# Kernel optimization log

Hardware: AMD Instinct MI355X
Metric: run time of the kernel (lower is better)

## Reference

```python
import jax, jax.numpy as jnp
import numpy as np

N, E, F_IN, H, G, C = 50000, 600000, 128, 128, 500, 10


def _lin(k, fi, fo):
    # Glorot-ish scaled init for a [fi, fo] weight
    return (jax.random.normal(k, (fi, fo), jnp.float32) / np.float32(np.sqrt(fi)))


def setup_inputs() -> dict:
    key = jax.random.key(0)
    ks = jax.random.split(key, 16)
    x = jax.random.normal(ks[0], (N, F_IN), jnp.float32)
    edge_index = jax.random.randint(ks[1], (2, E), 0, N, dtype=jnp.int32)
    batch = jnp.sort(jax.random.randint(ks[2], (N,), 0, G, dtype=jnp.int32))
    return {
        "x": x, "edge_index": edge_index, "batch": batch,
        # SAGEConv i: out = mean_aggr @ Wl + bl + x @ Wr  (PyG default: mean aggr, root weight, bias on lin_l)
        "Wl1": _lin(ks[3], F_IN, H), "bl1": jnp.zeros((H,), jnp.float32), "Wr1": _lin(ks[4], F_IN, H),
        "Wl2": _lin(ks[5], H, H),    "bl2": jnp.zeros((H,), jnp.float32), "Wr2": _lin(ks[6], H, H),
        "Wl3": _lin(ks[7], H, H),    "bl3": jnp.zeros((H,), jnp.float32), "Wr3": _lin(ks[8], H, H),
        "W4": _lin(ks[9], H, 64), "b4": jnp.zeros((64,), jnp.float32),
        "W5": _lin(ks[10], 64, C), "b5": jnp.zeros((C,), jnp.float32),
    }


def _segment_mean(vals, ids, num_segments):
    s = jax.ops.segment_sum(vals, ids, num_segments=num_segments)
    cnt = jax.ops.segment_sum(jnp.ones((vals.shape[0], 1), vals.dtype), ids, num_segments=num_segments)
    return s / jnp.maximum(cnt, 1.0)


def _sage_conv(x, src, dst, Wl, bl, Wr):
    # gather source features along edges, mean-aggregate at destinations
    aggr = _segment_mean(x[src], dst, N)  # [N, F]
    return aggr @ Wl + bl + x @ Wr


def reference(x, edge_index, batch, Wl1, bl1, Wr1, Wl2, bl2, Wr2, Wl3, bl3, Wr3, W4, b4, W5, b5):
    src, dst = edge_index[0], edge_index[1]
    h = jax.nn.relu(_sage_conv(x, src, dst, Wl1, bl1, Wr1))
    h = jax.nn.relu(_sage_conv(h, src, dst, Wl2, bl2, Wr2))
    h = jax.nn.relu(_sage_conv(h, src, dst, Wl3, bl3, Wr3))
    g = _segment_mean(h, batch, G)          # global mean pool -> [G, H]
    g = jax.nn.relu(g @ W4 + b4)
    return jax.nn.log_softmax(g @ W5 + b5, axis=-1)
```

## Files before the change

kernel.cpp:

```cpp
#include <hip/hip_runtime.h>
#include <hip/hip_bf16.h>
#include <math.h>

#define FH 128

typedef __attribute__((ext_vector_type(8))) short short8v;
typedef __attribute__((ext_vector_type(4))) float float4v;
typedef unsigned short ushort_t;
typedef unsigned int   uint32;

__device__ __forceinline__ ushort_t f2bf(float f) {
    uint32 u = __builtin_bit_cast(uint32, f);
    u += 0x7fffu + ((u >> 16) & 1u);
    return (ushort_t)(u >> 16);
}
__device__ __forceinline__ float bf_lo(uint32 w) { return __builtin_bit_cast(float, w << 16); }
__device__ __forceinline__ float bf_hi(uint32 w) { return __builtin_bit_cast(float, w & 0xffff0000u); }
__device__ __forceinline__ uint32 pack2(float lo, float hi) {
    return (uint32)f2bf(lo) | ((uint32)f2bf(hi) << 16);
}

__global__ __launch_bounds__(256) void zero_kernel(int* __restrict__ p, int n) {
    int i = (blockIdx.x * 256 + threadIdx.x) * 4;
    if (i + 3 < n) {
        *(int4*)(p + i) = make_int4(0, 0, 0, 0);
    } else {
        for (int j = i; j < n; ++j) p[j] = 0;
    }
}

__device__ __forceinline__ void pack_one(const float* __restrict__ Wl,
                                         const float* __restrict__ Wr,
                                         ushort_t* __restrict__ Bp, int t) {
    int k = t >> 7, n = t & 127;
    float v = (k < FH) ? Wl[k * FH + n] : Wr[(k - FH) * FH + n];
    int nt = n >> 4, kt = k >> 5;
    int lane = (n & 15) + (((k >> 3) & 3) << 4);
    int j = k & 7;
    Bp[(((nt * 8 + kt) * 64) + lane) * 8 + j] = f2bf(v);
}

__global__ __launch_bounds__(256) void fused_prep_kernel(
        const float* __restrict__ x, ushort_t* __restrict__ xb, size_t n, int cvtBlocks,
        const float* __restrict__ Wl1, const float* __restrict__ Wr1, ushort_t* __restrict__ Bp1,
        const float* __restrict__ Wl2, const float* __restrict__ Wr2, ushort_t* __restrict__ Bp2,
        const float* __restrict__ Wl3, const float* __restrict__ Wr3, ushort_t* __restrict__ Bp3,
        const int* __restrict__ dst, int* __restrict__ deg, int E, int degBlocks,
        const int* __restrict__ batch, int* __restrict__ gstart, int N, int G) {
    int b = blockIdx.x;
    if (b < cvtBlocks) {
        size_t base = ((size_t)b * 256 + threadIdx.x) * 8;
        if (base >= n) return;
        const float4 a = *(const float4*)(x + base);
        const float4 c = *(const float4*)(x + base + 4);
        ushort_t o[8] = {f2bf(a.x), f2bf(a.y), f2bf(a.z), f2bf(a.w),
                         f2bf(c.x), f2bf(c.y), f2bf(c.z), f2bf(c.w)};
        *(uint4*)(xb + base) = *(const uint4*)o;
        return;
    }
    b -= cvtBlocks;
    if (b < 384) {
        int which = b >> 7;
        int t = (b & 127) * 256 + threadIdx.x;
        if (which == 0)      pack_one(Wl1, Wr1, Bp1, t);
        else if (which == 1) pack_one(Wl2, Wr2, Bp2, t);
        else                 pack_one(Wl3, Wr3, Bp3, t);
        return;
    }
    b -= 384;
    if (b < degBlocks) {
        int e = b * 256 + threadIdx.x;
        if (e < E) atomicAdd(&deg[dst[e]], 1);
        return;
    }
    b -= degBlocks;
    {
        int g = b * 256 + threadIdx.x;
        if (g > G) return;
        int lo = 0, hi = N;
        while (lo < hi) {
            int mid = (lo + hi) >> 1;
            if (batch[mid] < g) lo = mid + 1; else hi = mid;
        }
        gstart[g] = lo;
    }
}

__global__ __launch_bounds__(256) void scan1_kernel(const int* __restrict__ deg,
                                                    int* __restrict__ rowptr,
                                                    int* __restrict__ blockSums, int N) {
    __shared__ int lds[256];
    const int base = blockIdx.x * 1024;
    const int t = threadIdx.x;
    int v[4]; int sum = 0;
    #pragma unroll
    for (int j = 0; j < 4; ++j) {
        int idx = base + t * 4 + j;
        v[j] = (idx < N) ? deg[idx] : 0;
        sum += v[j];
    }
    lds[t] = sum; __syncthreads();
    for (int off = 1; off < 256; off <<= 1) {
        int val = lds[t];
        int add = (t >= off) ? lds[t - off] : 0;
        __syncthreads();
        lds[t] = val + add;
        __syncthreads();
    }
    int run = (t > 0) ? lds[t - 1] : 0;
    #pragma unroll
    for (int j = 0; j < 4; ++j) {
        int idx = base + t * 4 + j;
        if (idx < N) rowptr[idx] = run;
        run += v[j];
    }
    if (t == 255) blockSums[blockIdx.x] = lds[255];
}

__global__ __launch_bounds__(256) void scan3_kernel(int* __restrict__ rowptr,
                                                    int* __restrict__ pos,
                                                    const int* __restrict__ blockSums,
                                                    int N, int nb) {
    __shared__ int sAdd, sTot;
    if (threadIdx.x < 64) {
        const int lane = threadIdx.x;
        const int bid = blockIdx.x;
        int pre = 0, tot = 0;
        for (int i = lane; i < nb; i += 64) {
            const int v = blockSums[i];
            tot += v;
            if (i < bid) pre += v;
        }
        #pragma unroll
        for (int off = 1; off < 64; off <<= 1) {
            pre += __shfl_xor(pre, off);
            tot += __shfl_xor(tot, off);
        }
        if (lane == 0) { sAdd = pre; sTot = tot; }
    }
    __syncthreads();
    const int add = sAdd;
    const int base = blockIdx.x * 1024;
    #pragma unroll
    for (int j = 0; j < 4; ++j) {
        int idx = base + threadIdx.x * 4 + j;
        if (idx < N) {
            int v = rowptr[idx] + add;
            rowptr[idx] = v;
            pos[idx] = v;
        }
    }
    if (blockIdx.x == (unsigned)(nb - 1) && threadIdx.x == 0) rowptr[N] = sTot;
}

__global__ __launch_bounds__(256) void fill_csr_kernel(const int* __restrict__ src,
                                                       const int* __restrict__ dst,
                                                       int* __restrict__ pos,
                                                       int* __restrict__ csr, int E) {
    int e = blockIdx.x * 256 + threadIdx.x;
    if (e >= E) return;
    int idx = atomicAdd(&pos[dst[e]], 1);
    csr[idx] = src[e];
}

__global__ __launch_bounds__(256) void pull_mean_kernel(const ushort_t* __restrict__ x,
                                                        const int* __restrict__ rowptr,
                                                        const int* __restrict__ csr,
                                                        ushort_t* __restrict__ aggr, int N) {
    const int v = (blockIdx.x * 256 + threadIdx.x) >> 6;
    if (v >= N) return;
    const int lane = threadIdx.x & 63;
    const int grp  = lane >> 4;
    const int li   = lane & 15;
    const int beg = rowptr[v], end = rowptr[v + 1];
    const uint4* xp = (const uint4*)x + li;

    const uint4 z = {0u, 0u, 0u, 0u};
    uint4 w0 = z, w1 = z, w2 = z, w3 = z;
    const int i0 = beg + grp;
    if (i0 < end)      w0 = xp[(size_t)csr[i0] * 16];
    if (i0 + 4 < end)  w1 = xp[(size_t)csr[i0 + 4] * 16];
    if (i0 + 8 < end)  w2 = xp[(size_t)csr[i0 + 8] * 16];
    if (i0 + 12 < end) w3 = xp[(size_t)csr[i0 + 12] * 16];

    float a0 = (bf_lo(w0.x) + bf_lo(w1.x)) + (bf_lo(w2.x) + bf_lo(w3.x));
    float a1 = (bf_hi(w0.x) + bf_hi(w1.x)) + (bf_hi(w2.x) + bf_hi(w3.x));
    float a2 = (bf_lo(w0.y) + bf_lo(w1.y)) + (bf_lo(w2.y) + bf_lo(w3.y));
    float a3 = (bf_hi(w0.y) + bf_hi(w1.y)) + (bf_hi(w2.y) + bf_hi(w3.y));
    float a4 = (bf_lo(w0.z) + bf_lo(w1.z)) + (bf_lo(w2.z) + bf_lo(w3.z));
    float a5 = (bf_hi(w0.z) + bf_hi(w1.z)) + (bf_hi(w2.z) + bf_hi(w3.z));
    float a6 = (bf_lo(w0.w) + bf_lo(w1.w)) + (bf_lo(w2.w) + bf_lo(w3.w));
    float a7 = (bf_hi(w0.w) + bf_hi(w1.w)) + (bf_hi(w2.w) + bf_hi(w3.w));

    for (int i = beg + 16 + grp; i < end; i += 4) {
        const uint4 w = xp[(size_t)csr[i] * 16];
        a0 += bf_lo(w.x); a1 += bf_hi(w.x); a2 += bf_lo(w.y); a3 += bf_hi(w.y);
        a4 += bf_lo(w.z); a5 += bf_hi(w.z); a6 += bf_lo(w.w); a7 += bf_hi(w.w);
    }

    a0 += __shfl_xor(a0, 16); a1 += __shfl_xor(a1, 16);
    a2 += __shfl_xor(a2, 16); a3 += __shfl_xor(a3, 16);
    a4 += __shfl_xor(a4, 16); a5 += __shfl_xor(a5, 16);
    a6 += __shfl_xor(a6, 16); a7 += __shfl_xor(a7, 16);
    a0 += __shfl_xor(a0, 32); a1 += __shfl_xor(a1, 32);
    a2 += __shfl_xor(a2, 32); a3 += __shfl_xor(a3, 32);
    a4 += __shfl_xor(a4, 32); a5 += __shfl_xor(a5, 32);
    a6 += __shfl_xor(a6, 32); a7 += __shfl_xor(a7, 32);

    if (grp == 0) {
        const float inv = 1.0f / (float)max(end - beg, 1);
        uint4 o;
        o.x = pack2(a0 * inv, a1 * inv);
        o.y = pack2(a2 * inv, a3 * inv);
        o.z = pack2(a4 * inv, a5 * inv);
        o.w = pack2(a6 * inv, a7 * inv);
        ((uint4*)aggr)[(size_t)v * 16 + li] = o;
    }
}

#define SO_STRIDE 136
__global__ __launch_bounds__(256) void sage_mfma_kernel(const ushort_t* __restrict__ xin,
                                                        const ushort_t* __restrict__ aggr,
                                                        const ushort_t* __restrict__ Bp,
                                                        const float* __restrict__ bl,
                                                        ushort_t* __restrict__ out, int M) {
    __shared__ ushort_t sB[16384];
    const int tid = threadIdx.x;
    const int wave = tid >> 6;
    const int lane = tid & 63;
    const int grp  = lane >> 4;
    const int li   = lane & 15;
    const int rowBase = (blockIdx.x * 4 + wave) * 16;
    const int arow = min(rowBase + li, M - 1);

    short8v afrag[8];
    #pragma unroll
    for (int kt = 0; kt < 4; ++kt)
        afrag[kt] = *(const short8v*)(aggr + (size_t)arow * FH + kt * 32 + grp * 8);
    #pragma unroll
    for (int kt = 0; kt < 4; ++kt)
        afrag[4 + kt] = *(const short8v*)(xin + (size_t)arow * FH + kt * 32 + grp * 8);

    float4v acc[8];
    #pragma unroll
    for (int ch = 0; ch < 2; ++ch) {
        if (ch) __syncthreads();
        {
            const uint4* s = (const uint4*)Bp + ch * 2048;
            uint4* d = (uint4*)sB;
            #pragma unroll
            for (int i = 0; i < 8; ++i)
                d[tid + 256 * i] = s[tid + 256 * i];
        }
        __syncthreads();
        #pragma unroll
        for (int ntl = 0; ntl < 4; ++ntl) {
            const int nt = ch * 4 + ntl;
            acc[nt] = (float4v){0.f, 0.f, 0.f, 0.f};
            #pragma unroll
            for (int kt = 0; kt < 8; ++kt) {
                const short8v b = *(const short8v*)(sB + (((ntl * 8 + kt) * 64) + lane) * 8);
                acc[nt] = __builtin_amdgcn_mfma_f32_16x16x32_bf16(afrag[kt], b, acc[nt], 0, 0, 0);
            }
        }
    }

    __syncthreads();

    ushort_t* so = sB + wave * (16 * SO_STRIDE);
    #pragma unroll
    for (int nt = 0; nt < 8; ++nt) {
        const float bias = bl[nt * 16 + li];
        #pragma unroll
        for (int r = 0; r < 4; ++r)
            so[(grp * 4 + r) * SO_STRIDE + nt * 16 + li] = f2bf(fmaxf(acc[nt][r] + bias, 0.f));
    }
    #pragma unroll
    for (int t = 0; t < 4; ++t) {
        const int idx = lane + 64 * t;
        const int r  = idx >> 4;
        const int ch = idx & 15;
        const int row = rowBase + r;
        if (row < M) {
            const uint4 val = *(const uint4*)(so + r * SO_STRIDE + ch * 8);
            *(uint4*)(out + (size_t)row * FH + ch * 8) = val;
        }
    }
}

__global__ __launch_bounds__(256) void head_kernel(const ushort_t* __restrict__ h,
                                                   const int* __restrict__ gstart,
                                                   const float* __restrict__ W4,
                                                   const float* __restrict__ b4,
                                                   const float* __restrict__ W5,
                                                   const float* __restrict__ b5,
                                                   float* __restrict__ out, int G) {
    __shared__ float sred[4][FH];
    __shared__ float sg2[64];
    __shared__ float sl[10];
    __shared__ float slse;
    const int g = blockIdx.x;
    const int t = threadIdx.x;
    const int wave = t >> 6, lane = t & 63;
    const int beg = gstart[g], end = gstart[g + 1];

    const uint32* hp = (const uint32*)h + lane;
    float a0 = 0.f, a1 = 0.f;
    for (int i = beg + wave; i < end; i += 4) {
        const uint32 w = hp[(size_t)i * 64];
        a0 += bf_lo(w); a1 += bf_hi(w);
    }
    sred[wave][lane * 2]     = a0;
    sred[wave][lane * 2 + 1] = a1;
    __syncthreads();
    if (t < FH) {
        const float s = sred[0][t] + sred[1][t] + sred[2][t] + sred[3][t];
        sred[0][t] = s / (float)max(end - beg, 1);
    }
    __syncthreads();
    if (t < 64) {
        float acc = b4[t];
        #pragma unroll 4
        for (int k = 0; k < FH; ++k)
            acc += sred[0][k] * W4[k * 64 + t];
        sg2[t] = fmaxf(acc, 0.f);
    }
    __syncthreads();
    if (t < 10) {
        float acc = b5[t];
        #pragma unroll 4
        for (int k = 0; k < 64; ++k)
            acc += sg2[k] * W5[k * 10 + t];
        sl[t] = acc;
    }
    __syncthreads();
    if (t == 0) {
        float m = sl[0];
        #pragma unroll
        for (int j = 1; j < 10; ++j) m = fmaxf(m, sl[j]);
        float s = 0.f;
        #pragma unroll
        for (int j = 0; j < 10; ++j) s += expf(sl[j] - m);
        slse = m + logf(s);
    }
    __syncthreads();
    if (t < 10) out[g * 10 + t] = sl[t] - slse;
}

extern "C" void kernel_launch(void* const* d_in, const int* in_sizes, int n_in,
                              void* d_out, int out_size, void* d_ws, size_t ws_size,
                              hipStream_t stream) {
    const float* x     = (const float*)d_in[0];
    const int*   ei    = (const int*)d_in[1];
    const int*   batch = (const int*)d_in[2];
    const float* Wl1 = (const float*)d_in[3];
    const float* bl1 = (const float*)d_in[4];
    const float* Wr1 = (const float*)d_in[5];
    const float* Wl2 = (const float*)d_in[6];
    const float* bl2 = (const float*)d_in[7];
    const float* Wr2 = (const float*)d_in[8];
    const float* Wl3 = (const float*)d_in[9];
    const float* bl3 = (const float*)d_in[10];
    const float* Wr3 = (const float*)d_in[11];
    const float* W4  = (const float*)d_in[12];
    const float* b4  = (const float*)d_in[13];
    const float* W5  = (const float*)d_in[14];
    const float* b5  = (const float*)d_in[15];
    float* out = (float*)d_out;

    const int N = in_sizes[0] / FH;
    const int E = in_sizes[1] / 2;
    const int G = out_size / 10;
    const int* src = ei;
    const int* dst = ei + E;

    char* p = (char*)d_ws;
    auto take = [&](size_t bytes) { char* q = p; p += (bytes + 255) & ~(size_t)255; return q; };
    ushort_t* xb    = (ushort_t*)take((size_t)N * FH * 2);
    ushort_t* h     = (ushort_t*)take((size_t)N * FH * 2);
    ushort_t* aggrb = (ushort_t*)take((size_t)N * FH * 2);
    int* deg        = (int*)take((size_t)N * 4);
    int* rowptr     = (int*)take((size_t)(N + 1) * 4);
    int* pos        = (int*)take((size_t)N * 4);
    int* csr        = (int*)take((size_t)E * 4);
    int* blockSums  = (int*)take(256 * 4);
    ushort_t* Bp1   = (ushort_t*)take(256 * FH * 2);
    ushort_t* Bp2   = (ushort_t*)take(256 * FH * 2);
    ushort_t* Bp3   = (ushort_t*)take(256 * FH * 2);
    int* gstart     = (int*)take((size_t)(G + 1) * 4);

    const int nb = (N + 1023) / 1024;

    zero_kernel<<<(N / 4 + 255) / 256, 256, 0, stream>>>(deg, N);

    const int cvtBlocks = (int)(((size_t)N * FH / 8 + 255) / 256);
    const int degBlocks = (E + 255) / 256;
    const int gbBlocks  = (G + 1 + 255) / 256;
    fused_prep_kernel<<<cvtBlocks + 384 + degBlocks + gbBlocks, 256, 0, stream>>>(
        x, xb, (size_t)N * FH, cvtBlocks,
        Wl1, Wr1, Bp1, Wl2, Wr2, Bp2, Wl3, Wr3, Bp3,
        dst, deg, E, degBlocks,
        batch, gstart, N, G);

    scan1_kernel<<<nb, 256, 0, stream>>>(deg, rowptr, blockSums, N);
    scan3_kernel<<<nb, 256, 0, stream>>>(rowptr, pos, blockSums, N, nb);
    fill_csr_kernel<<<(E + 255) / 256, 256, 0, stream>>>(src, dst, pos, csr, E);

    const int pullGrid = (N * 64 + 255) / 256;
    const int gemmGrid = (N + 63) / 64;

    pull_mean_kernel<<<pullGrid, 256, 0, stream>>>(xb, rowptr, csr, aggrb, N);
    sage_mfma_kernel<<<gemmGrid, 256, 0, stream>>>(xb, aggrb, Bp1, bl1, h, N);

    pull_mean_kernel<<<pullGrid, 256, 0, stream>>>(h, rowptr, csr, aggrb, N);
    sage_mfma_kernel<<<gemmGrid, 256, 0, stream>>>(h, aggrb, Bp2, bl2, h, N);

    pull_mean_kernel<<<pullGrid, 256, 0, stream>>>(h, rowptr, csr, aggrb, N);
    sage_mfma_kernel<<<gemmGrid, 256, 0, stream>>>(h, aggrb, Bp3, bl3, h, N);

    head_kernel<<<G, 256, 0, stream>>>(h, gstart, W4, b4, W5, b5, out, G);
}
```

Baseline: 221.4 us.

## Restructure CSR build, widen gather unroll, and stage full weight matrix in LDS

Moves the degree atomics out of the prep kernel into a dedicated kernel, and folds the graph-start binary search into the second scan kernel. The CSR fill now handles two edges per thread using vectorized int2 loads. The neighbor gather issues six independent row loads up front instead of four. The MFMA GEMM loads the entire packed weight matrix into a 64KB LDS buffer once, instead of in two chunks with extra barriers, at the cost of higher LDS use per block and possibly lower occupancy.

After: 218.9 us. No clear change (-1.1%).

```diff
diff --git a/kernel.cpp b/kernel.cpp
--- a/kernel.cpp
+++ b/kernel.cpp
@@ -40,13 +40,11 @@
     Bp[(((nt * 8 + kt) * 64) + lane) * 8 + j] = f2bf(v);
 }
 
-__global__ __launch_bounds__(256) void fused_prep_kernel(
+__global__ __launch_bounds__(256) void prep_kernel(
         const float* __restrict__ x, ushort_t* __restrict__ xb, size_t n, int cvtBlocks,
         const float* __restrict__ Wl1, const float* __restrict__ Wr1, ushort_t* __restrict__ Bp1,
         const float* __restrict__ Wl2, const float* __restrict__ Wr2, ushort_t* __restrict__ Bp2,
-        const float* __restrict__ Wl3, const float* __restrict__ Wr3, ushort_t* __restrict__ Bp3,
-        const int* __restrict__ dst, int* __restrict__ deg, int E, int degBlocks,
-        const int* __restrict__ batch, int* __restrict__ gstart, int N, int G) {
+        const float* __restrict__ Wl3, const float* __restrict__ Wr3, ushort_t* __restrict__ Bp3) {
     int b = blockIdx.x;
     if (b < cvtBlocks) {
         size_t base = ((size_t)b * 256 + threadIdx.x) * 8;
@@ -59,31 +57,19 @@
         return;
     }
     b -= cvtBlocks;
-    if (b < 384) {
+    {
         int which = b >> 7;
         int t = (b & 127) * 256 + threadIdx.x;
         if (which == 0)      pack_one(Wl1, Wr1, Bp1, t);
         else if (which == 1) pack_one(Wl2, Wr2, Bp2, t);
         else                 pack_one(Wl3, Wr3, Bp3, t);
-        return;
-    }
-    b -= 384;
-    if (b < degBlocks) {
-        int e = b * 256 + threadIdx.x;
-        if (e < E) atomicAdd(&deg[dst[e]], 1);
-        return;
-    }
-    b -= degBlocks;
-    {
-        int g = b * 256 + threadIdx.x;
-        if (g > G) return;
-        int lo = 0, hi = N;
-        while (lo < hi) {
-            int mid = (lo + hi) >> 1;
-            if (batch[mid] < g) lo = mid + 1; else hi = mid;
-        }
-        gstart[g] = lo;
-    }
+    }
+}
+
+__global__ __launch_bounds__(256) void deg_kernel(const int* __restrict__ dst,
+                                                  int* __restrict__ deg, int E) {
+    int e = blockIdx.x * 256 + threadIdx.x;
+    if (e < E) atomicAdd(&deg[dst[e]], 1);
 }
 
 __global__ __launch_bounds__(256) void scan1_kernel(const int* __restrict__ deg,
@@ -117,10 +103,23 @@
     if (t == 255) blockSums[blockIdx.x] = lds[255];
 }
 
-__global__ __launch_bounds__(256) void scan3_kernel(int* __restrict__ rowptr,
-                                                    int* __restrict__ pos,
-                                                    const int* __restrict__ blockSums,
-                                                    int N, int nb) {
+__global__ __launch_bounds__(256) void scan3_gb_kernel(int* __restrict__ rowptr,
+                                                       int* __restrict__ pos,
+                                                       const int* __restrict__ blockSums,
+                                                       int N, int nb,
+                                                       const int* __restrict__ batch,
+                                                       int* __restrict__ gstart, int G) {
+    if ((int)blockIdx.x >= nb) {
+        int g = ((int)blockIdx.x - nb) * 256 + threadIdx.x;
+        if (g > G) return;
+        int lo = 0, hi = N;
+        while (lo < hi) {
+            int mid = (lo + hi) >> 1;
+            if (batch[mid] < g) lo = mid + 1; else hi = mid;
+        }
+        gstart[g] = lo;
+        return;
+    }
     __shared__ int sAdd, sTot;
     if (threadIdx.x < 64) {
         const int lane = threadIdx.x;
@@ -157,10 +156,19 @@
                                                        const int* __restrict__ dst,
                                                        int* __restrict__ pos,
                                                        int* __restrict__ csr, int E) {
-    int e = blockIdx.x * 256 + threadIdx.x;
+    int e = (blockIdx.x * 256 + threadIdx.x) * 2;
     if (e >= E) return;
-    int idx = atomicAdd(&pos[dst[e]], 1);
-    csr[idx] = src[e];
+    if (e + 1 < E) {
+        const int2 s2 = *(const int2*)(src + e);
+        const int2 d2 = *(const int2*)(dst + e);
+        int i0 = atomicAdd(&pos[d2.x], 1);
+        int i1 = atomicAdd(&pos[d2.y], 1);
+        csr[i0] = s2.x;
+        csr[i1] = s2.y;
+    } else {
+        int idx = atomicAdd(&pos[dst[e]], 1);
+        csr[idx] = src[e];
+    }
 }
 
 __global__ __launch_bounds__(256) void pull_mean_kernel(const ushort_t* __restrict__ x,
@@ -176,23 +184,25 @@
     const uint4* xp = (const uint4*)x + li;
 
     const uint4 z = {0u, 0u, 0u, 0u};
-    uint4 w0 = z, w1 = z, w2 = z, w3 = z;
+    uint4 w0 = z, w1 = z, w2 = z, w3 = z, w4 = z, w5 = z;
     const int i0 = beg + grp;
     if (i0 < end)      w0 = xp[(size_t)csr[i0] * 16];
     if (i0 + 4 < end)  w1 = xp[(size_t)csr[i0 + 4] * 16];
     if (i0 + 8 < end)  w2 = xp[(size_t)csr[i0 + 8] * 16];
     if (i0 + 12 < end) w3 = xp[(size_t)csr[i0 + 12] * 16];
-
-    float a0 = (bf_lo(w0.x) + bf_lo(w1.x)) + (bf_lo(w2.x) + bf_lo(w3.x));
-    float a1 = (bf_hi(w0.x) + bf_hi(w1.x)) + (bf_hi(w2.x) + bf_hi(w3.x));
-    float a2 = (bf_lo(w0.y) + bf_lo(w1.y)) + (bf_lo(w2.y) + bf_lo(w3.y));
-    float a3 = (bf_hi(w0.y) + bf_hi(w1.y)) + (bf_hi(w2.y) + bf_hi(w3.y));
-    float a4 = (bf_lo(w0.z) + bf_lo(w1.z)) + (bf_lo(w2.z) + bf_lo(w3.z));
-    float a5 = (bf_hi(w0.z) + bf_hi(w1.z)) + (bf_hi(w2.z) + bf_hi(w3.z));
-    float a6 = (bf_lo(w0.w) + bf_lo(w1.w)) + (bf_lo(w2.w) + bf_lo(w3.w));
-    float a7 = (bf_hi(w0.w) + bf_hi(w1.w)) + (bf_hi(w2.w) + bf_hi(w3.w));
-
-    for (int i = beg + 16 + grp; i < end; i += 4) {
+    if (i0 + 16 < end) w4 = xp[(size_t)csr[i0 + 16] * 16];
+    if (i0 + 20 < end) w5 = xp[(size_t)csr[i0 + 20] * 16];
+
+    float a0 = (bf_lo(w0.x) + bf_lo(w1.x)) + (bf_lo(w2.x) + bf_lo(w3.x)) + (bf_lo(w4.x) + bf_lo(w5.x));
+    float a1 = (bf_hi(w0.x) + bf_hi(w1.x)) + (bf_hi(w2.x) + bf_hi(w3.x)) + (bf_hi(w4.x) + bf_hi(w5.x));
+    float a2 = (bf_lo(w0.y) + bf_lo(w1.y)) + (bf_lo(w2.y) + bf_lo(w3.y)) + (bf_lo(w4.y) + bf_lo(w5.y));
+    float a3 = (bf_hi(w0.y) + bf_hi(w1.y)) + (bf_hi(w2.y) + bf_hi(w3.y)) + (bf_hi(w4.y) + bf_hi(w5.y));
+    float a4 = (bf_lo(w0.z) + bf_lo(w1.z)) + (bf_lo(w2.z) + bf_lo(w3.z)) + (bf_lo(w4.z) + bf_lo(w5.z));
+    float a5 = (bf_hi(w0.z) + bf_hi(w1.z)) + (bf_hi(w2.z) + bf_hi(w3.z)) + (bf_hi(w4.z) + bf_hi(w5.z));
+    float a6 = (bf_lo(w0.w) + bf_lo(w1.w)) + (bf_lo(w2.w) + bf_lo(w3.w)) + (bf_lo(w4.w) + bf_lo(w5.w));
+    float a7 = (bf_hi(w0.w) + bf_hi(w1.w)) + (bf_hi(w2.w) + bf_hi(w3.w)) + (bf_hi(w4.w) + bf_hi(w5.w));
+
+    for (int i = beg + 24 + grp; i < end; i += 4) {
         const uint4 w = xp[(size_t)csr[i] * 16];
         a0 += bf_lo(w.x); a1 += bf_hi(w.x); a2 += bf_lo(w.y); a3 += bf_hi(w.y);
         a4 += bf_lo(w.z); a5 += bf_hi(w.z); a6 += bf_lo(w.w); a7 += bf_hi(w.w);
@@ -224,8 +234,17 @@
                                                         const ushort_t* __restrict__ Bp,
                                                         const float* __restrict__ bl,
                                                         ushort_t* __restrict__ out, int M) {
-    __shared__ ushort_t sB[16384];
+    __shared__ ushort_t sB[32768];
     const int tid = threadIdx.x;
+    {
+        const uint4* s = (const uint4*)Bp;
+        uint4* d = (uint4*)sB;
+        #pragma unroll
+        for (int i = 0; i < 16; ++i)
+            d[tid + 256 * i] = s[tid + 256 * i];
+    }
+    __syncthreads();
+
     const int wave = tid >> 6;
     const int lane = tid & 63;
     const int grp  = lane >> 4;
@@ -243,25 +262,12 @@
 
     float4v acc[8];
     #pragma unroll
-    for (int ch = 0; ch < 2; ++ch) {
-        if (ch) __syncthreads();
-        {
-            const uint4* s = (const uint4*)Bp + ch * 2048;
-            uint4* d = (uint4*)sB;
-            #pragma unroll
-            for (int i = 0; i < 8; ++i)
-                d[tid + 256 * i] = s[tid + 256 * i];
-        }
-        __syncthreads();
-        #pragma unroll
-        for (int ntl = 0; ntl < 4; ++ntl) {
-            const int nt = ch * 4 + ntl;
-            acc[nt] = (float4v){0.f, 0.f, 0.f, 0.f};
-            #pragma unroll
-            for (int kt = 0; kt < 8; ++kt) {
-                const short8v b = *(const short8v*)(sB + (((ntl * 8 + kt) * 64) + lane) * 8);
-                acc[nt] = __builtin_amdgcn_mfma_f32_16x16x32_bf16(afrag[kt], b, acc[nt], 0, 0, 0);
-            }
+    for (int nt = 0; nt < 8; ++nt) {
+        acc[nt] = (float4v){0.f, 0.f, 0.f, 0.f};
+        #pragma unroll
+        for (int kt = 0; kt < 8; ++kt) {
+            const short8v b = *(const short8v*)(sB + (((nt * 8 + kt) * 64) + lane) * 8);
+            acc[nt] = __builtin_amdgcn_mfma_f32_16x16x32_bf16(afrag[kt], b, acc[nt], 0, 0, 0);
         }
     }
 
@@ -394,17 +400,17 @@
     zero_kernel<<<(N / 4 + 255) / 256, 256, 0, stream>>>(deg, N);
 
     const int cvtBlocks = (int)(((size_t)N * FH / 8 + 255) / 256);
-    const int degBlocks = (E + 255) / 256;
-    const int gbBlocks  = (G + 1 + 255) / 256;
-    fused_prep_kernel<<<cvtBlocks + 384 + degBlocks + gbBlocks, 256, 0, stream>>>(
+    prep_kernel<<<cvtBlocks + 384, 256, 0, stream>>>(
         x, xb, (size_t)N * FH, cvtBlocks,
-        Wl1, Wr1, Bp1, Wl2, Wr2, Bp2, Wl3, Wr3, Bp3,
-        dst, deg, E, degBlocks,
-        batch, gstart, N, G);
-
+        Wl1, Wr1, Bp1, Wl2, Wr2, Bp2, Wl3, Wr3, Bp3);
+
+    deg_kernel<<<(E + 255) / 256, 256, 0, stream>>>(dst, deg, E);
+
+    const int gbBlocks = (G + 1 + 255) / 256;
     scan1_kernel<<<nb, 256, 0, stream>>>(deg, rowptr, blockSums, N);
-    scan3_kernel<<<nb, 256, 0, stream>>>(rowptr, pos, blockSums, N, nb);
-    fill_csr_kernel<<<(E + 255) / 256, 256, 0, stream>>>(src, dst, pos, csr, E);
+    scan3_gb_kernel<<<nb + gbBlocks, 256, 0, stream>>>(rowptr, pos, blockSums, N, nb,
+                                                       batch, gstart, G);
+    fill_csr_kernel<<<(E / 2 + 255) / 256, 256, 0, stream>>>(src, dst, pos, csr, E);
 
     const int pullGrid = (N * 64 + 255) / 256;
     const int gemmGrid = (N + 63) / 64;
```
